# Kernel optimization log

Measured on AMD Instinct MI355X. Metric: run time of the kernel, lower is better.

The kernel has to match this reference:

```python
import jax, jax.numpy as jnp
import numpy as np

S1, S2 = 1024, 1024
DA, DV, DOUT = 2, 64, 1
K1, K2 = 32, 32


def _gelu(x):
    # torch nn.GELU() default is the exact erf-based gelu
    return jax.nn.gelu(x, approximate=False)


def _flayer(Rr, Ri, w, x):
    f = jnp.fft.rfftn(x, axes=(0, 1))[:K1, :K2]            # [K1,K2,DV] complex
    Rf = jnp.einsum('abc,abcd->abd', f, Rr + 1j * Ri)       # [K1,K2,DV] complex
    kernelpart = jnp.fft.irfftn(Rf, s=(S1, S2), axes=(0, 1))  # [S1,S2,DV] real
    return _gelu(kernelpart + x @ w)


def setup_inputs() -> dict:
    key = jax.random.key(0)
    ks = jax.random.split(key, 20)
    d = {}
    d['input'] = jax.random.normal(ks[0], (S1, S2, DA), dtype=jnp.float32)
    d['Wsh'] = jax.random.normal(ks[1], (DA, DV), dtype=jnp.float32) * (1.0 / np.sqrt(DA))
    d['bsh'] = jax.random.normal(ks[2], (DV,), dtype=jnp.float32) * 0.02
    for i, base in zip(range(1, 5), range(3, 15, 3)):
        d[f'Rr{i}'] = jax.random.normal(ks[base], (K1, K2, DV, DV), dtype=jnp.float32) * (1.0 / DV)
        d[f'Ri{i}'] = jax.random.normal(ks[base + 1], (K1, K2, DV, DV), dtype=jnp.float32) * (1.0 / DV)
        d[f'w{i}'] = jax.random.normal(ks[base + 2], (DV, DV), dtype=jnp.float32) * (1.0 / np.sqrt(DV))
    d['Wp'] = jax.random.normal(ks[15], (DV, DOUT), dtype=jnp.float32) * (1.0 / np.sqrt(DV))
    d['bp'] = jax.random.normal(ks[16], (DOUT,), dtype=jnp.float32) * 0.02
    return d


def reference(input, Wsh, bsh, Rr1, Ri1, w1, Rr2, Ri2, w2,
              Rr3, Ri3, w3, Rr4, Ri4, w4, Wp, bp):
    vt = _gelu(input @ Wsh + bsh)          # Shallow: Linear + GELU
    vt = _flayer(Rr1, Ri1, w1, vt)
    vt = _flayer(Rr2, Ri2, w2, vt)
    vt = _flayer(Rr3, Ri3, w3, vt)
    vt = _flayer(Rr4, Ri4, w4, vt)
    u = (vt @ Wp + bp)[:, :, 0]            # Project, take channel 0 -> [S1,S2]
    return u
```

## Files before the change

kernel.cpp:

```cpp
#include <hip/hip_runtime.h>
#include <math.h>

#define MASKN 1023

typedef unsigned short ushort_t;
typedef __attribute__((ext_vector_type(8))) short short8;
typedef __attribute__((ext_vector_type(4))) float floatx4;
typedef __attribute__((ext_vector_type(4))) unsigned short us4v;

__device__ __forceinline__ float gelu_f(float x) {
    float x2 = x * x;
    float inner = fmaf(0.044715f * x, x2, x);
    float t = exp2f(inner * -2.302089214f);
    return x * __builtin_amdgcn_rcpf(1.0f + t);
}

__device__ __forceinline__ float bf2f(ushort_t h) {
    return __uint_as_float(((unsigned int)h) << 16);
}
__device__ __forceinline__ ushort_t f2bf(float f) {
    unsigned int u = __float_as_uint(f);
    u += 0x7FFFu + ((u >> 16) & 1u);
    return (ushort_t)(u >> 16);
}
struct us4 { ushort_t x, y, z, w; };

__device__ __forceinline__ unsigned int pk2bf(float lo, float hi) {
    unsigned int r;
    asm("v_cvt_pk_bf16_f32 %0, %1, %2" : "=v"(r) : "v"(lo), "v"(hi));
    return r;
}

__device__ __forceinline__ void st4(ushort_t* p, float4 v) {
    uint2 w;
    w.x = pk2bf(v.x, v.y);
    w.y = pk2bf(v.z, v.w);
    *(uint2*)p = w;
}

__device__ __forceinline__ void async16(ushort_t* l, const ushort_t* g) {
    __builtin_amdgcn_global_load_lds(
        (const __attribute__((address_space(1))) void*)g,
        (__attribute__((address_space(3))) void*)l, 16, 0, 0);
}

__global__ void k_fill_tw(float* __restrict__ ct, float* __restrict__ st) {
    int j = blockIdx.x * 256 + threadIdx.x;
    float ang = (float)j * (6.283185307179586f / 1024.0f);
    float s, c;
    sincosf(ang, &s, &c);
    ct[j] = c; st[j] = s;
}

__global__ void k_fill_T1(ushort_t* __restrict__ T1h, ushort_t* __restrict__ T1l) {
    int idx = blockIdx.x * 256 + threadIdx.x;
    int k2p = idx >> 10, y = idx & 1023;
    int k2 = k2p >> 1;
    float ang = (float)((k2 * y) & MASKN) * (6.283185307179586f / 1024.0f);
    float s, c;
    sincosf(ang, &s, &c);
    float v = (k2p & 1) ? -s : c;
    ushort_t h = f2bf(v);
    T1h[idx] = h;
    T1l[idx] = f2bf(v - bf2f(h));
}

__global__ void k_fill_T2(ushort_t* __restrict__ T2h, ushort_t* __restrict__ T2l) {
    int idx = blockIdx.x * 256 + threadIdx.x;
    int n2 = idx >> 6, kk = idx & 63;
    int k2 = kk >> 1;
    float ang = (float)((k2 * n2) & MASKN) * (6.283185307179586f / 1024.0f);
    float s, c;
    sincosf(ang, &s, &c);
    float v = (kk & 1) ? -s : c;
    ushort_t h = f2bf(v);
    T2h[idx] = h;
    T2l[idx] = f2bf(v - bf2f(h));
}

__global__ void k_fill_wT(const float* __restrict__ w1, const float* __restrict__ w2,
        const float* __restrict__ w3, const float* __restrict__ w4,
        ushort_t* __restrict__ wTh, ushort_t* __restrict__ wTl) {
    int l = blockIdx.y;
    int i = blockIdx.x * 256 + threadIdx.x;
    int d = i >> 6, c = i & 63;
    const float* w = (l == 0) ? w1 : (l == 1) ? w2 : (l == 2) ? w3 : w4;
    float v = w[c * 64 + d];
    ushort_t h = f2bf(v);
    wTh[l * 4096 + i] = h;
    wTl[l * 4096 + i] = f2bf(v - bf2f(h));
}

__global__ __launch_bounds__(256) void k_shallow(const float* __restrict__ in,
        const float* __restrict__ Wsh, const float* __restrict__ bsh,
        ushort_t* __restrict__ vt) {
    int tid = blockIdx.x * 256 + threadIdx.x;
    int p = tid >> 4, c0 = (tid & 15) << 2;
    float a0 = in[p * 2], a1 = in[p * 2 + 1];
    float4 w0 = *(const float4*)&Wsh[c0];
    float4 w1 = *(const float4*)&Wsh[64 + c0];
    float4 b  = *(const float4*)&bsh[c0];
    float4 r;
    r.x = gelu_f(fmaf(a0, w0.x, fmaf(a1, w1.x, b.x)));
    r.y = gelu_f(fmaf(a0, w0.y, fmaf(a1, w1.y, b.y)));
    r.z = gelu_f(fmaf(a0, w0.z, fmaf(a1, w1.z, b.z)));
    r.w = gelu_f(fmaf(a0, w0.w, fmaf(a1, w1.w, b.w)));
    st4(&vt[(size_t)p * 64 + c0], r);
}

#define VS1 72
__global__ __launch_bounds__(256, 3) void k_f1(const ushort_t* __restrict__ vt,
        const ushort_t* __restrict__ T1h, const ushort_t* __restrict__ T1l,
        float* __restrict__ gT) {
    __shared__ __align__(16) ushort_t t1s[2][8192];
    __shared__ __align__(16) ushort_t vs[2][64 * VS1];
    int t = threadIdx.x;
    int x0 = blockIdx.x * 2;
    int wv = t >> 6, lane = t & 63;
    int lm = lane & 15, quad = lane >> 4;
    int lrow = t & 63, cq = (t >> 6) * 16;
    const ushort_t* vrow0 = vt + (size_t)x0 * 65536;
    const ushort_t* vrow1 = vrow0 + 65536;

    floatx4 acc[2][4];
    #pragma unroll
    for (int xi = 0; xi < 2; ++xi)
        #pragma unroll
        for (int nt = 0; nt < 4; ++nt) acc[xi][nt] = (floatx4)(0.f);

    uint4 pf[2][2][2];
    #pragma unroll
    for (int i = 0; i < 4; ++i) {
        int j = (wv * 4 + i) * 64 + lane;
        int jj = j & 511;
        int r = jj >> 3, du = jj & 7, su = du ^ (r & 7);
        const ushort_t* src = ((j < 512) ? T1h : T1l) + (size_t)r * 1024 + su * 8;
        async16(&t1s[0][(wv * 4 + i) * 512], src);
    }
    __builtin_amdgcn_sched_barrier(0);
    {
        const ushort_t* s00 = vrow0 + (size_t)lrow * 64 + cq;
        pf[0][0][0] = *(const uint4*)(s00);
        pf[0][0][1] = *(const uint4*)(s00 + 8);
        const ushort_t* s01 = vrow1 + (size_t)lrow * 64 + cq;
        pf[0][1][0] = *(const uint4*)(s01);
        pf[0][1][1] = *(const uint4*)(s01 + 8);
        const ushort_t* s10 = vrow0 + (size_t)(64 + lrow) * 64 + cq;
        pf[1][0][0] = *(const uint4*)(s10);
        pf[1][0][1] = *(const uint4*)(s10 + 8);
        const ushort_t* s11 = vrow1 + (size_t)(64 + lrow) * 64 + cq;
        pf[1][1][0] = *(const uint4*)(s11);
        pf[1][1][1] = *(const uint4*)(s11 + 8);
    }
    __builtin_amdgcn_sched_barrier(0);

    for (int hc = 0; hc < 16; ++hc) {
        int b = hc & 1;
        #pragma unroll
        for (int xi = 0; xi < 2; ++xi)
            #pragma unroll
            for (int i = 0; i < 2; ++i) {
                union { uint4 u; ushort_t e[8]; } uv;
                uv.u = pf[b][xi][i];
                #pragma unroll
                for (int j = 0; j < 8; ++j)
                    vs[xi][(cq + i * 8 + j) * VS1 + lrow] = uv.e[j];
            }
        __builtin_amdgcn_sched_barrier(0);
        if (hc < 15) asm volatile("s_waitcnt vmcnt(4)" ::: "memory");
        else         asm volatile("s_waitcnt vmcnt(0)" ::: "memory");
        __builtin_amdgcn_sched_barrier(0);
        __builtin_amdgcn_s_barrier();
        if (hc < 15) {
            #pragma unroll
            for (int i = 0; i < 4; ++i) {
                int j = (wv * 4 + i) * 64 + lane;
                int jj = j & 511;
                int r = jj >> 3, du = jj & 7, su = du ^ (r & 7);
                const ushort_t* src = ((j < 512) ? T1h : T1l)
                                      + (size_t)r * 1024 + (hc + 1) * 64 + su * 8;
                async16(&t1s[b ^ 1][(wv * 4 + i) * 512], src);
            }
        }
        if (hc < 14) {
            const ushort_t* s0 = vrow0 + (size_t)((hc + 2) * 64 + lrow) * 64 + cq;
            pf[b][0][0] = *(const uint4*)(s0);
            pf[b][0][1] = *(const uint4*)(s0 + 8);
            const ushort_t* s1 = vrow1 + (size_t)((hc + 2) * 64 + lrow) * 64 + cq;
            pf[b][1][0] = *(const uint4*)(s1);
            pf[b][1][1] = *(const uint4*)(s1 + 8);
        }
        __builtin_amdgcn_sched_barrier(0);

        #pragma unroll
        for (int ys = 0; ys < 2; ++ys) {
            short8 af0 = *(const short8*)&vs[0][(wv * 16 + lm) * VS1 + ys * 32 + quad * 8];
            short8 af1 = *(const short8*)&vs[1][(wv * 16 + lm) * VS1 + ys * 32 + quad * 8];
            #pragma unroll
            for (int nt = 0; nt < 4; ++nt) {
                int sl = (((ys * 4 + quad) ^ (lm & 7)) * 8);
                short8 bh = *(const short8*)&t1s[b][(nt * 16 + lm) * 64 + sl];
                short8 bl = *(const short8*)&t1s[b][4096 + (nt * 16 + lm) * 64 + sl];
                acc[0][nt] = __builtin_amdgcn_mfma_f32_16x16x32_bf16(af0, bh, acc[0][nt], 0, 0, 0);
                acc[0][nt] = __builtin_amdgcn_mfma_f32_16x16x32_bf16(af0, bl, acc[0][nt], 0, 0, 0);
                acc[1][nt] = __builtin_amdgcn_mfma_f32_16x16x32_bf16(af1, bh, acc[1][nt], 0, 0, 0);
                acc[1][nt] = __builtin_amdgcn_mfma_f32_16x16x32_bf16(af1, bl, acc[1][nt], 0, 0, 0);
            }
        }
    }
    #pragma unroll
    for (int xi = 0; xi < 2; ++xi) {
        float* grow = gT + (size_t)(x0 + xi) * 4096;
        #pragma unroll
        for (int nt = 0; nt < 4; ++nt)
            #pragma unroll
            for (int r = 0; r < 4; ++r)
                grow[(wv * 16 + quad * 4 + r) * 64 + nt * 16 + lm] = acc[xi][nt][r];
    }
}

__global__ __launch_bounds__(256) void k_f2(const float* __restrict__ gT,
        const float* __restrict__ ct, const float* __restrict__ st,
        float* __restrict__ fpr, float* __restrict__ fpi) {
    int t = threadIdx.x;
    int cx = blockIdx.x;
    int cg = blockIdx.y;
    int k10 = blockIdx.z * 8;
    int l = t & 63;
    int q = t >> 6;
    int c = cg * 4 + q;
    int e = l & 1;
    int k2 = l >> 1;
    float acc[8];
    #pragma unroll
    for (int i = 0; i < 8; ++i) acc[i] = 0.f;
    for (int xi = 0; xi < 128; ++xi) {
        int x = cx * 128 + xi;
        float v = gT[(size_t)x * 4096 + c * 64 + l];
        float p = __shfl_xor(v, 1);
        float gr = e ? p : v;
        float gi = e ? v : p;
        float u  = e ? gi : gr;
        float w2 = e ? -gr : gi;
        float cb = ct[x], sb = st[x];
        int ph = (x * k10) & MASKN;
        float cr = ct[ph], sr = st[ph];
        #pragma unroll
        for (int j = 0; j < 8; ++j) {
            acc[j] = fmaf(u, cr, fmaf(w2, sr, acc[j]));
            float nc = fmaf(cr, cb, -sr * sb);
            float ns = fmaf(sr, cb, cr * sb);
            cr = nc; sr = ns;
        }
    }
    float* dst = e ? fpi : fpr;
    #pragma unroll
    for (int j = 0; j < 8; ++j)
        dst[(size_t)cx * 65536 + ((k10 + j) * 32 + k2) * 64 + c] = acc[j];
}

__global__ __launch_bounds__(64) void k_mix(const float* __restrict__ fpr, const float* __restrict__ fpi,
        const float* __restrict__ Rr, const float* __restrict__ Ri,
        float* __restrict__ Rfr, float* __restrict__ Rfi) {
    __shared__ float fr[64], fi[64];
    int m = blockIdx.x;
    int d = threadIdx.x;
    float sr = 0.f, si = 0.f;
    #pragma unroll
    for (int ch = 0; ch < 8; ++ch) {
        sr += fpr[(size_t)ch * 65536 + m * 64 + d];
        si += fpi[(size_t)ch * 65536 + m * 64 + d];
    }
    fr[d] = sr; fi[d] = si;
    __syncthreads();
    const float* Rrb = Rr + (size_t)m * 4096;
    const float* Rib = Ri + (size_t)m * 4096;
    float ar = 0.f, ai = 0.f;
    for (int c = 0; c < 64; ++c) {
        float rr = Rrb[c * 64 + d], ri = Rib[c * 64 + d];
        ar = fmaf(fr[c], rr, fmaf(-fi[c], ri, ar));
        ai = fmaf(fr[c], ri, fmaf(fi[c], rr, ai));
    }
    Rfr[m * 64 + d] = ar;
    Rfi[m * 64 + d] = ai;
}

__global__ __launch_bounds__(256) void k_i1(const float* __restrict__ Rfr, const float* __restrict__ Rfi,
        const float* __restrict__ ctg, const float* __restrict__ stg,
        ushort_t* __restrict__ Bh, ushort_t* __restrict__ Bl) {
    __shared__ float ct[1024], st[1024];
    int t = threadIdx.x;
    #pragma unroll
    for (int i = 0; i < 4; ++i) { int j = t + 256 * i; ct[j] = ctg[j]; st[j] = stg[j]; }
    __syncthreads();
    int n1 = blockIdx.x;
    int d = t & 63;
    int k20 = (t >> 6) * 8;
    float br[8], bi[8];
    #pragma unroll
    for (int j = 0; j < 8; ++j) { br[j] = 0.f; bi[j] = 0.f; }
    int idx = 0;
    for (int k1 = 0; k1 < 32; ++k1) {
        float cc = ct[idx], ss = st[idx];
        idx = (idx + n1) & MASKN;
        #pragma unroll
        for (int j = 0; j < 8; ++j) {
            float rr = Rfr[(k1 * 32 + k20 + j) * 64 + d];
            float ri = Rfi[(k1 * 32 + k20 + j) * 64 + d];
            br[j] = fmaf(rr, cc, fmaf(-ri, ss, br[j]));
            bi[j] = fmaf(rr, ss, fmaf(ri, cc, bi[j]));
        }
    }
    union { uint4 u[2]; ushort_t e[16]; } hh, ll;
    #pragma unroll
    for (int j = 0; j < 8; ++j) {
        int k2 = k20 + j;
        float sc = (k2 == 0 ? 1.0f : 2.0f) * 9.5367431640625e-7f;
        float vr = br[j] * sc, vi = bi[j] * sc;
        ushort_t hr = f2bf(vr), hi2 = f2bf(vi);
        hh.e[2 * j] = hr;          hh.e[2 * j + 1] = hi2;
        ll.e[2 * j] = f2bf(vr - bf2f(hr));
        ll.e[2 * j + 1] = f2bf(vi - bf2f(hi2));
    }
    size_t base = ((size_t)n1 * 64 + d) * 64 + 2 * k20;
    *(uint4*)(Bh + base) = hh.u[0];
    *(uint4*)(Bh + base + 8) = hh.u[1];
    *(uint4*)(Bl + base) = ll.u[0];
    *(uint4*)(Bl + base + 8) = ll.u[1];
}

template<bool FINAL>
__global__ __launch_bounds__(256, 4) void k_i2(ushort_t* __restrict__ vt,
        const ushort_t* __restrict__ Bh, const ushort_t* __restrict__ Bl,
        const ushort_t* __restrict__ T2h, const ushort_t* __restrict__ T2l,
        const ushort_t* __restrict__ wTh, const ushort_t* __restrict__ wTl,
        const float* __restrict__ Wp, const float* __restrict__ bp,
        float* __restrict__ out) {
    __shared__ __align__(16) ushort_t ab[16384];
    int t = threadIdx.x;
    int wv = t >> 6, lane = t & 63;
    int lm = lane & 15, quad = lane >> 4;
    int n1 = blockIdx.x;
    const ushort_t* Bhr = Bh + (size_t)n1 * 4096;
    const ushort_t* Blr = Bl + (size_t)n1 * 4096;

    {
        const ushort_t* s = (wv == 0) ? Bhr : (wv == 1) ? Blr : (wv == 2) ? wTh : wTl;
        #pragma unroll
        for (int i = 0; i < 8; ++i) {
            int j = i * 64 + lane;
            int r = j >> 3, u = (j & 7) ^ (r & 7);
            async16(&ab[wv * 4096 + i * 512], s + r * 64 + u * 8);
        }
    }

    int n2b = wv * 16 + lm;
    const ushort_t* t2hp = T2h + n2b * 64 + quad * 8;
    const ushort_t* t2lp = T2l + n2b * 64 + quad * 8;
    const ushort_t* vrd  = vt + ((size_t)n1 * 1024 + n2b) * 64 + quad * 8;
    ushort_t*       vst  = vt + ((size_t)n1 * 1024 + n2b) * 64;

    short8 th[2][2], tl[2][2], vv[2][2];
    #pragma unroll
    for (int ks = 0; ks < 2; ++ks) {
        th[0][ks] = *(const short8*)(t2hp + ks * 32);
        tl[0][ks] = *(const short8*)(t2lp + ks * 32);
        vv[0][ks] = *(const short8*)(vrd + ks * 32);
    }
    float4 wpv[4];
    float bp0 = 0.f;
    if (FINAL) {
        bp0 = bp[0];
        #pragma unroll
        for (int mt = 0; mt < 4; ++mt) wpv[mt] = *(const float4*)&Wp[mt * 16 + quad * 4];
    }
    __syncthreads();

    int r7 = lm & 7;
    #pragma unroll
    for (int c = 0; c < 16; ++c) {
        if (c < 15) {
            #pragma unroll
            for (int ks = 0; ks < 2; ++ks) {
                th[(c + 1) & 1][ks] = *(const short8*)(t2hp + (c + 1) * 4096 + ks * 32);
                tl[(c + 1) & 1][ks] = *(const short8*)(t2lp + (c + 1) * 4096 + ks * 32);
                vv[(c + 1) & 1][ks] = *(const short8*)(vrd + (size_t)(c + 1) * 4096 + ks * 32);
            }
        }
        __builtin_amdgcn_sched_barrier(0);

        floatx4 acc[4];
        #pragma unroll
        for (int mt = 0; mt < 4; ++mt) acc[mt] = (floatx4)(0.f);

        __builtin_amdgcn_s_setprio(1);
        #pragma unroll
        for (int ks = 0; ks < 2; ++ks) {
            int sl = ((ks * 4 + quad) ^ r7) * 8;
            #pragma unroll
            for (int mt = 0; mt < 4; ++mt) {
                int ro = (mt * 16 + lm) * 64 + sl;
                short8 ah = *(const short8*)&ab[ro];
                short8 al = *(const short8*)&ab[4096 + ro];
                short8 wh = *(const short8*)&ab[8192 + ro];
                short8 wl = *(const short8*)&ab[12288 + ro];
                acc[mt] = __builtin_amdgcn_mfma_f32_16x16x32_bf16(ah, th[c & 1][ks], acc[mt], 0, 0, 0);
                acc[mt] = __builtin_amdgcn_mfma_f32_16x16x32_bf16(al, th[c & 1][ks], acc[mt], 0, 0, 0);
                acc[mt] = __builtin_amdgcn_mfma_f32_16x16x32_bf16(ah, tl[c & 1][ks], acc[mt], 0, 0, 0);
                acc[mt] = __builtin_amdgcn_mfma_f32_16x16x32_bf16(wh, vv[c & 1][ks], acc[mt], 0, 0, 0);
                acc[mt] = __builtin_amdgcn_mfma_f32_16x16x32_bf16(wl, vv[c & 1][ks], acc[mt], 0, 0, 0);
            }
        }
        __builtin_amdgcn_s_setprio(0);

        if (!FINAL) {
            #pragma unroll
            for (int mt = 0; mt < 4; ++mt) {
                uint2 w;
                w.x = pk2bf(gelu_f(acc[mt][0]), gelu_f(acc[mt][1]));
                w.y = pk2bf(gelu_f(acc[mt][2]), gelu_f(acc[mt][3]));
                *(uint2*)(vst + (size_t)c * 4096 + mt * 16 + quad * 4) = w;
            }
        } else {
            float s = 0.f;
            #pragma unroll
            for (int mt = 0; mt < 4; ++mt) {
                s = fmaf(gelu_f(acc[mt][0]), wpv[mt].x, s);
                s = fmaf(gelu_f(acc[mt][1]), wpv[mt].y, s);
                s = fmaf(gelu_f(acc[mt][2]), wpv[mt].z, s);
                s = fmaf(gelu_f(acc[mt][3]), wpv[mt].w, s);
            }
            s += __shfl_xor(s, 16);
            s += __shfl_xor(s, 32);
            if (quad == 0)
                out[(size_t)n1 * 1024 + c * 64 + n2b] = s + bp0;
        }
    }
}

extern "C" void kernel_launch(void* const* d_in, const int* in_sizes, int n_in,
                              void* d_out, int out_size, void* d_ws, size_t ws_size,
                              hipStream_t stream) {
    const float* in  = (const float*)d_in[0];
    const float* Wsh = (const float*)d_in[1];
    const float* bsh = (const float*)d_in[2];
    const float* Wp  = (const float*)d_in[15];
    const float* bp  = (const float*)d_in[16];

    char* wsb = (char*)d_ws;
    ushort_t* vt   = (ushort_t*)wsb;
    float* ctab = (float*)(wsb + 134217728);
    float* stab = ctab + 1024;
    float* gT   = stab + 1024;
    float* Rfr  = gT + 4194304;
    float* Rfi  = Rfr + 65536;
    ushort_t* T1h = (ushort_t*)(Rfi + 65536);
    ushort_t* T1l = T1h + 65536;
    ushort_t* T2h = T1l + 65536;
    ushort_t* T2l = T2h + 65536;
    ushort_t* wTh = T2l + 65536;
    ushort_t* wTl = wTh + 16384;
    ushort_t* Bh  = (ushort_t*)gT;
    ushort_t* Bl  = Bh + 4194304;
    float* fpr = (float*)d_out;
    float* fpi = fpr + 524288;

    k_fill_tw<<<4, 256, 0, stream>>>(ctab, stab);
    k_fill_T1<<<256, 256, 0, stream>>>(T1h, T1l);
    k_fill_T2<<<256, 256, 0, stream>>>(T2h, T2l);
    k_fill_wT<<<dim3(16, 4), 256, 0, stream>>>((const float*)d_in[5], (const float*)d_in[8],
                                               (const float*)d_in[11], (const float*)d_in[14], wTh, wTl);
    k_shallow<<<65536, 256, 0, stream>>>(in, Wsh, bsh, vt);
    for (int L = 0; L < 4; ++L) {
        const float* Rr = (const float*)d_in[3 + L * 3];
        const float* Ri = (const float*)d_in[4 + L * 3];
        k_f1<<<512, 256, 0, stream>>>(vt, T1h, T1l, gT);
        k_f2<<<dim3(8, 16, 4), 256, 0, stream>>>(gT, ctab, stab, fpr, fpi);
        k_mix<<<1024, 64, 0, stream>>>(fpr, fpi, Rr, Ri, Rfr, Rfi);
        k_i1<<<1024, 256, 0, stream>>>(Rfr, Rfi, ctab, stab, Bh, Bl);
        if (L < 3) {
            k_i2<false><<<1024, 256, 0, stream>>>(vt, Bh, Bl, T2h, T2l,
                    wTh + L * 4096, wTl + L * 4096, nullptr, nullptr, nullptr);
        } else {
            k_i2<true><<<1024, 256, 0, stream>>>(vt, Bh, Bl, T2h, T2l,
                    wTh + L * 4096, wTl + L * 4096, Wp, bp, (float*)d_out);
        }
    }
}
```

Before: 736.3 us.

## Fuse next layer's forward DFT stage into inverse-transform epilogue kernel

The inverse-transform kernel for layers 1-3 now also performs the first forward DFT stage (previously k_f1) of the following layer. It transposes the freshly computed GELU tile through shared memory and multiplies it against T1 twiddles with MFMA, accumulating into gT. Only the initial k_f1 runs standalone, which removes three launches and three re-reads of vt. The B buffers are interleaved per row so hi and lo parts sit together. The cost is more LDS, occupancy lowered to 2 blocks per CU, extra barriers per chunk, and an aliasing hazard because gT shares storage with Bhl while the kernel reads Bhl and writes gT.

```diff
diff --git a/kernel.cpp b/kernel.cpp
--- a/kernel.cpp
+++ b/kernel.cpp
@@ -287,7 +287,7 @@
 
 __global__ __launch_bounds__(256) void k_i1(const float* __restrict__ Rfr, const float* __restrict__ Rfi,
         const float* __restrict__ ctg, const float* __restrict__ stg,
-        ushort_t* __restrict__ Bh, ushort_t* __restrict__ Bl) {
+        ushort_t* __restrict__ Bhl) {
     __shared__ float ct[1024], st[1024];
     int t = threadIdx.x;
     #pragma unroll
@@ -322,27 +322,28 @@
         ll.e[2 * j] = f2bf(vr - bf2f(hr));
         ll.e[2 * j + 1] = f2bf(vi - bf2f(hi2));
     }
-    size_t base = ((size_t)n1 * 64 + d) * 64 + 2 * k20;
-    *(uint4*)(Bh + base) = hh.u[0];
-    *(uint4*)(Bh + base + 8) = hh.u[1];
-    *(uint4*)(Bl + base) = ll.u[0];
-    *(uint4*)(Bl + base + 8) = ll.u[1];
-}
-
-template<bool FINAL>
-__global__ __launch_bounds__(256, 4) void k_i2(ushort_t* __restrict__ vt,
-        const ushort_t* __restrict__ Bh, const ushort_t* __restrict__ Bl,
+    size_t base = (size_t)n1 * 8192 + d * 64 + 2 * k20;
+    *(uint4*)(Bhl + base) = hh.u[0];
+    *(uint4*)(Bhl + base + 8) = hh.u[1];
+    *(uint4*)(Bhl + 4096 + base) = ll.u[0];
+    *(uint4*)(Bhl + 4096 + base + 8) = ll.u[1];
+}
+
+__global__ __launch_bounds__(256, 2) void k_i2f(ushort_t* __restrict__ vt,
+        ushort_t* Bhl,
         const ushort_t* __restrict__ T2h, const ushort_t* __restrict__ T2l,
         const ushort_t* __restrict__ wTh, const ushort_t* __restrict__ wTl,
-        const float* __restrict__ Wp, const float* __restrict__ bp,
-        float* __restrict__ out) {
+        const ushort_t* __restrict__ T1h, const ushort_t* __restrict__ T1l,
+        float* gT) {
     __shared__ __align__(16) ushort_t ab[16384];
+    __shared__ __align__(16) ushort_t t1s[8192];
+    __shared__ __align__(16) ushort_t trans[64 * VS1];
     int t = threadIdx.x;
     int wv = t >> 6, lane = t & 63;
     int lm = lane & 15, quad = lane >> 4;
     int n1 = blockIdx.x;
-    const ushort_t* Bhr = Bh + (size_t)n1 * 4096;
-    const ushort_t* Blr = Bl + (size_t)n1 * 4096;
+    const ushort_t* Bhr = Bhl + (size_t)n1 * 8192;
+    const ushort_t* Blr = Bhr + 4096;
 
     {
         const ushort_t* s = (wv == 0) ? Bhr : (wv == 1) ? Blr : (wv == 2) ? wTh : wTl;
@@ -367,18 +368,24 @@
         tl[0][ks] = *(const short8*)(t2lp + ks * 32);
         vv[0][ks] = *(const short8*)(vrd + ks * 32);
     }
-    float4 wpv[4];
-    float bp0 = 0.f;
-    if (FINAL) {
-        bp0 = bp[0];
-        #pragma unroll
-        for (int mt = 0; mt < 4; ++mt) wpv[mt] = *(const float4*)&Wp[mt * 16 + quad * 4];
-    }
+    floatx4 facc[4];
+    #pragma unroll
+    for (int nt = 0; nt < 4; ++nt) facc[nt] = (floatx4)(0.f);
     __syncthreads();
 
     int r7 = lm & 7;
     #pragma unroll
     for (int c = 0; c < 16; ++c) {
+        #pragma unroll
+        for (int i = 0; i < 4; ++i) {
+            int j = (wv * 4 + i) * 64 + lane;
+            int jj = j & 511;
+            int rr_ = jj >> 3, du = jj & 7, su = du ^ (rr_ & 7);
+            const ushort_t* src = ((j < 512) ? T1h : T1l)
+                                  + (size_t)rr_ * 1024 + c * 64 + su * 8;
+            async16(&t1s[(wv * 4 + i) * 512], src);
+        }
+        __builtin_amdgcn_sched_barrier(0);
         if (c < 15) {
             #pragma unroll
             for (int ks = 0; ks < 2; ++ks) {
@@ -392,7 +399,6 @@
         floatx4 acc[4];
         #pragma unroll
         for (int mt = 0; mt < 4; ++mt) acc[mt] = (floatx4)(0.f);
-
         __builtin_amdgcn_s_setprio(1);
         #pragma unroll
         for (int ks = 0; ks < 2; ++ks) {
@@ -413,28 +419,139 @@
         }
         __builtin_amdgcn_s_setprio(0);
 
-        if (!FINAL) {
+        uint2 w[4];
+        #pragma unroll
+        for (int mt = 0; mt < 4; ++mt) {
+            w[mt].x = pk2bf(gelu_f(acc[mt][0]), gelu_f(acc[mt][1]));
+            w[mt].y = pk2bf(gelu_f(acc[mt][2]), gelu_f(acc[mt][3]));
+            *(uint2*)(vst + (size_t)c * 4096 + mt * 16 + quad * 4) = w[mt];
+        }
+        #pragma unroll
+        for (int mt = 0; mt < 4; ++mt) {
+            int chb = mt * 16 + quad * 4;
+            trans[(chb + 0) * VS1 + n2b] = (ushort_t)(w[mt].x & 0xffffu);
+            trans[(chb + 1) * VS1 + n2b] = (ushort_t)(w[mt].x >> 16);
+            trans[(chb + 2) * VS1 + n2b] = (ushort_t)(w[mt].y & 0xffffu);
+            trans[(chb + 3) * VS1 + n2b] = (ushort_t)(w[mt].y >> 16);
+        }
+        __builtin_amdgcn_sched_barrier(0);
+        asm volatile("s_waitcnt lgkmcnt(0)" ::: "memory");
+        if (c < 15) asm volatile("s_waitcnt vmcnt(10)" ::: "memory");
+        else        asm volatile("s_waitcnt vmcnt(4)" ::: "memory");
+        __builtin_amdgcn_sched_barrier(0);
+        __builtin_amdgcn_s_barrier();
+        __builtin_amdgcn_sched_barrier(0);
+
+        #pragma unroll
+        for (int ys = 0; ys < 2; ++ys) {
+            short8 af = *(const short8*)&trans[(wv * 16 + lm) * VS1 + ys * 32 + quad * 8];
+            #pragma unroll
+            for (int nt = 0; nt < 4; ++nt) {
+                int sl = ((ys * 4 + quad) ^ r7) * 8;
+                short8 bh = *(const short8*)&t1s[(nt * 16 + lm) * 64 + sl];
+                short8 bl = *(const short8*)&t1s[4096 + (nt * 16 + lm) * 64 + sl];
+                facc[nt] = __builtin_amdgcn_mfma_f32_16x16x32_bf16(af, bh, facc[nt], 0, 0, 0);
+                facc[nt] = __builtin_amdgcn_mfma_f32_16x16x32_bf16(af, bl, facc[nt], 0, 0, 0);
+            }
+        }
+        __builtin_amdgcn_sched_barrier(0);
+        __builtin_amdgcn_s_barrier();
+        __builtin_amdgcn_sched_barrier(0);
+    }
+
+    float* grow = gT + (size_t)n1 * 4096;
+    #pragma unroll
+    for (int nt = 0; nt < 4; ++nt)
+        #pragma unroll
+        for (int r = 0; r < 4; ++r)
+            grow[(wv * 16 + quad * 4 + r) * 64 + nt * 16 + lm] = facc[nt][r];
+}
+
+__global__ __launch_bounds__(256, 4) void k_i2fin(ushort_t* __restrict__ vt,
+        const ushort_t* __restrict__ Bhl,
+        const ushort_t* __restrict__ T2h, const ushort_t* __restrict__ T2l,
+        const ushort_t* __restrict__ wTh, const ushort_t* __restrict__ wTl,
+        const float* __restrict__ Wp, const float* __restrict__ bp,
+        float* __restrict__ out) {
+    __shared__ __align__(16) ushort_t ab[16384];
+    int t = threadIdx.x;
+    int wv = t >> 6, lane = t & 63;
+    int lm = lane & 15, quad = lane >> 4;
+    int n1 = blockIdx.x;
+    const ushort_t* Bhr = Bhl + (size_t)n1 * 8192;
+    const ushort_t* Blr = Bhr + 4096;
+    {
+        const ushort_t* s = (wv == 0) ? Bhr : (wv == 1) ? Blr : (wv == 2) ? wTh : wTl;
+        #pragma unroll
+        for (int i = 0; i < 8; ++i) {
+            int j = i * 64 + lane;
+            int r = j >> 3, u = (j & 7) ^ (r & 7);
+            async16(&ab[wv * 4096 + i * 512], s + r * 64 + u * 8);
+        }
+    }
+    int n2b = wv * 16 + lm;
+    const ushort_t* t2hp = T2h + n2b * 64 + quad * 8;
+    const ushort_t* t2lp = T2l + n2b * 64 + quad * 8;
+    const ushort_t* vrd  = vt + ((size_t)n1 * 1024 + n2b) * 64 + quad * 8;
+    short8 th[2][2], tl[2][2], vv[2][2];
+    #pragma unroll
+    for (int ks = 0; ks < 2; ++ks) {
+        th[0][ks] = *(const short8*)(t2hp + ks * 32);
+        tl[0][ks] = *(const short8*)(t2lp + ks * 32);
+        vv[0][ks] = *(const short8*)(vrd + ks * 32);
+    }
+    float4 wpv[4];
+    float bp0 = bp[0];
+    #pragma unroll
+    for (int mt = 0; mt < 4; ++mt) wpv[mt] = *(const float4*)&Wp[mt * 16 + quad * 4];
+    __syncthreads();
+
+    int r7 = lm & 7;
+    #pragma unroll
+    for (int c = 0; c < 16; ++c) {
+        if (c < 15) {
+            #pragma unroll
+            for (int ks = 0; ks < 2; ++ks) {
+                th[(c + 1) & 1][ks] = *(const short8*)(t2hp + (c + 1) * 4096 + ks * 32);
+                tl[(c + 1) & 1][ks] = *(const short8*)(t2lp + (c + 1) * 4096 + ks * 32);
+                vv[(c + 1) & 1][ks] = *(const short8*)(vrd + (size_t)(c + 1) * 4096 + ks * 32);
+            }
+        }
+        __builtin_amdgcn_sched_barrier(0);
+        floatx4 acc[4];
+        #pragma unroll
+        for (int mt = 0; mt < 4; ++mt) acc[mt] = (floatx4)(0.f);
+        __builtin_amdgcn_s_setprio(1);
+        #pragma unroll
+        for (int ks = 0; ks < 2; ++ks) {
+            int sl = ((ks * 4 + quad) ^ r7) * 8;
             #pragma unroll
             for (int mt = 0; mt < 4; ++mt) {
-                uint2 w;
-                w.x = pk2bf(gelu_f(acc[mt][0]), gelu_f(acc[mt][1]));
-                w.y = pk2bf(gelu_f(acc[mt][2]), gelu_f(acc[mt][3]));
-                *(uint2*)(vst + (size_t)c * 4096 + mt * 16 + quad * 4) = w;
-            }
-        } else {
-            float s = 0.f;
-            #pragma unroll
-            for (int mt = 0; mt < 4; ++mt) {
-                s = fmaf(gelu_f(acc[mt][0]), wpv[mt].x, s);
-                s = fmaf(gelu_f(acc[mt][1]), wpv[mt].y, s);
-                s = fmaf(gelu_f(acc[mt][2]), wpv[mt].z, s);
-                s = fmaf(gelu_f(acc[mt][3]), wpv[mt].w, s);
-            }
-            s += __shfl_xor(s, 16);
-            s += __shfl_xor(s, 32);
-            if (quad == 0)
-                out[(size_t)n1 * 1024 + c * 64 + n2b] = s + bp0;
-        }
+                int ro = (mt * 16 + lm) * 64 + sl;
+                short8 ah = *(const short8*)&ab[ro];
+                short8 al = *(const short8*)&ab[4096 + ro];
+                short8 wh = *(const short8*)&ab[8192 + ro];
+                short8 wl = *(const short8*)&ab[12288 + ro];
+                acc[mt] = __builtin_amdgcn_mfma_f32_16x16x32_bf16(ah, th[c & 1][ks], acc[mt], 0, 0, 0);
+                acc[mt] = __builtin_amdgcn_mfma_f32_16x16x32_bf16(al, th[c & 1][ks], acc[mt], 0, 0, 0);
+                acc[mt] = __builtin_amdgcn_mfma_f32_16x16x32_bf16(ah, tl[c & 1][ks], acc[mt], 0, 0, 0);
+                acc[mt] = __builtin_amdgcn_mfma_f32_16x16x32_bf16(wh, vv[c & 1][ks], acc[mt], 0, 0, 0);
+                acc[mt] = __builtin_amdgcn_mfma_f32_16x16x32_bf16(wl, vv[c & 1][ks], acc[mt], 0, 0, 0);
+            }
+        }
+        __builtin_amdgcn_s_setprio(0);
+        float s = 0.f;
+        #pragma unroll
+        for (int mt = 0; mt < 4; ++mt) {
+            s = fmaf(gelu_f(acc[mt][0]), wpv[mt].x, s);
+            s = fmaf(gelu_f(acc[mt][1]), wpv[mt].y, s);
+            s = fmaf(gelu_f(acc[mt][2]), wpv[mt].z, s);
+            s = fmaf(gelu_f(acc[mt][3]), wpv[mt].w, s);
+        }
+        s += __shfl_xor(s, 16);
+        s += __shfl_xor(s, 32);
+        if (quad == 0)
+            out[(size_t)n1 * 1024 + c * 64 + n2b] = s + bp0;
     }
 }
 
@@ -460,8 +577,7 @@
     ushort_t* T2l = T2h + 65536;
     ushort_t* wTh = T2l + 65536;
     ushort_t* wTl = wTh + 16384;
-    ushort_t* Bh  = (ushort_t*)gT;
-    ushort_t* Bl  = Bh + 4194304;
+    ushort_t* Bhl = (ushort_t*)gT;
     float* fpr = (float*)d_out;
     float* fpi = fpr + 524288;
 
@@ -471,18 +587,18 @@
     k_fill_wT<<<dim3(16, 4), 256, 0, stream>>>((const float*)d_in[5], (const float*)d_in[8],
                                                (const float*)d_in[11], (const float*)d_in[14], wTh, wTl);
     k_shallow<<<65536, 256, 0, stream>>>(in, Wsh, bsh, vt);
+    k_f1<<<512, 256, 0, stream>>>(vt, T1h, T1l, gT);
     for (int L = 0; L < 4; ++L) {
         const float* Rr = (const float*)d_in[3 + L * 3];
         const float* Ri = (const float*)d_in[4 + L * 3];
-        k_f1<<<512, 256, 0, stream>>>(vt, T1h, T1l, gT);
         k_f2<<<dim3(8, 16, 4), 256, 0, stream>>>(gT, ctab, stab, fpr, fpi);
         k_mix<<<1024, 64, 0, stream>>>(fpr, fpi, Rr, Ri, Rfr, Rfi);
-        k_i1<<<1024, 256, 0, stream>>>(Rfr, Rfi, ctab, stab, Bh, Bl);
+        k_i1<<<1024, 256, 0, stream>>>(Rfr, Rfi, ctab, stab, Bhl);
         if (L < 3) {
-            k_i2<false><<<1024, 256, 0, stream>>>(vt, Bh, Bl, T2h, T2l,
-                    wTh + L * 4096, wTl + L * 4096, nullptr, nullptr, nullptr);
+            k_i2f<<<1024, 256, 0, stream>>>(vt, Bhl, T2h, T2l,
+                    wTh + L * 4096, wTl + L * 4096, T1h, T1l, gT);
         } else {
-            k_i2<true><<<1024, 256, 0, stream>>>(vt, Bh, Bl, T2h, T2l,
+            k_i2fin<<<1024, 256, 0, stream>>>(vt, Bhl, T2h, T2l,
                     wTh + L * 4096, wTl + L * 4096, Wp, bp, (float*)d_out);
         }
     }
```

Result: faster. 713.2 us (median of 2 runs) (-3.1%).
